# Performance work log

Measured on AMD Instinct MI355X. Metric: run time of the kernel, lower is better.

Reference implementation:

```python
import jax, jax.numpy as jnp
import numpy as np

B, C, L, M, F, N = 4, 32, 256, 256, 8, 64  # N = L // 4 per build()


def setup_inputs() -> dict:
    key = jax.random.key(0)
    k1, k2, k3, k4 = jax.random.split(key, 4)
    return {
        "x_real": jax.random.normal(k1, (B, 1, C, L, M), dtype=jnp.float32),
        "x_imag": jax.random.normal(k2, (B, 1, C, L, M), dtype=jnp.float32),
        "w_real": jax.random.normal(k3, (F, C, N, 1), dtype=jnp.float32),
        "w_imag": jax.random.normal(k4, (F, C, N, 1), dtype=jnp.float32),
    }


def _interp_weights(w, L):
    """tfp.math.interp_regular_1d_grid along axis=-2: map x_targ=0..L-1 over
    ref range [0, L-1] onto an N-point regular grid, linear interpolation."""
    Nn = w.shape[-2]
    t = jnp.arange(L, dtype=jnp.float32) / (L - 1) * (Nn - 1)  # grid coords
    lo = jnp.clip(jnp.floor(t).astype(jnp.int32), 0, Nn - 2)
    frac = (t - lo.astype(jnp.float32))[:, None]               # (L, 1)
    return w[:, :, lo, :] * (1.0 - frac) + w[:, :, lo + 1, :] * frac  # (F,C,L,1)


def reference(x_real, x_imag, w_real, w_imag):
    Lm = x_real.shape[-2]
    wr = _interp_weights(w_real, Lm)  # (F, C, L, 1)
    wi = _interp_weights(w_imag, Lm)
    # complex multiply: (wr + i*wi) * (xr + i*xi), broadcast (B,1,C,L,M)->(B,F,C,L,M)
    pr = wr * x_real - wi * x_imag
    pi = wr * x_imag + wi * x_real
    scale = jnp.sqrt(1.0 + jnp.arange(Lm, dtype=jnp.float32))[:, None]  # self.l, (L,1)
    yr = jnp.mean(pr, axis=-3) * scale  # (B, F, L, M)
    yi = jnp.mean(pi, axis=-3) * scale
    yr = jax.nn.relu(yr)  # relu=True: relu applied to real part only
    return jnp.stack([yr, yi])  # (2, B, F, L, M) == (real, imag)
```

## Files before the change

### kernel.cpp

```cpp
#include <hip/hip_runtime.h>
#include <math.h>

constexpr int B_ = 4, C_ = 32, L_ = 256, M_ = 256, F_ = 8, N_ = 64;

__global__ __launch_bounds__(128, 4) void sphereconv_kernel(
    const float* __restrict__ xr, const float* __restrict__ xi,
    const float* __restrict__ wr, const float* __restrict__ wi,
    float* __restrict__ out)
{
    __shared__ float ws[C_ * 16];

    const int b   = blockIdx.x >> 8;
    const int l   = blockIdx.x & (L_ - 1);
    const int tid = threadIdx.x;

    const float t = ((float)l / (float)(L_ - 1)) * (float)(N_ - 1);
    int lo = (int)floorf(t);
    if (lo > N_ - 2) lo = N_ - 2;
    const float frac = t - (float)lo;

#pragma unroll
    for (int i = tid; i < C_ * 16; i += 128) {
        const int c = i >> 4;
        const int j = i & 15;
        const int f = j & 7;
        const float* w = (j & 8) ? wi : wr;
        const int base = (f * C_ + c) * N_ + lo;
        ws[c * 16 + j] = w[base] * (1.0f - frac) + w[base + 1] * frac;
    }
    __syncthreads();

    float2 accr[F_], acci[F_];
#pragma unroll
    for (int f = 0; f < F_; ++f) {
        accr[f] = make_float2(0.f, 0.f);
        acci[f] = make_float2(0.f, 0.f);
    }

    const size_t strideC2 = (size_t)L_ * M_ / 2;
    const size_t xoff = ((size_t)b * C_) * L_ * M_ + (size_t)l * M_ + tid * 2;
    const float2* xr2 = (const float2*)(xr + xoff);
    const float2* xi2 = (const float2*)(xi + xoff);

#define CX(f, A, Bv)                                          \
    accr[f].x = fmaf(A, vr.x, fmaf(-(Bv), vi.x, accr[f].x));  \
    accr[f].y = fmaf(A, vr.y, fmaf(-(Bv), vi.y, accr[f].y));  \
    acci[f].x = fmaf(A, vi.x, fmaf((Bv), vr.x, acci[f].x));   \
    acci[f].y = fmaf(A, vi.y, fmaf((Bv), vr.y, acci[f].y));

#pragma unroll 4
    for (int c = 0; c < C_; ++c) {
        const float2 vr = xr2[c * strideC2];
        const float2 vi = xi2[c * strideC2];
        const float4 a0 = *(const float4*)&ws[c * 16 + 0];
        const float4 a1 = *(const float4*)&ws[c * 16 + 4];
        const float4 b0 = *(const float4*)&ws[c * 16 + 8];
        const float4 b1 = *(const float4*)&ws[c * 16 + 12];
        CX(0, a0.x, b0.x)
        CX(1, a0.y, b0.y)
        CX(2, a0.z, b0.z)
        CX(3, a0.w, b0.w)
        CX(4, a1.x, b1.x)
        CX(5, a1.y, b1.y)
        CX(6, a1.z, b1.z)
        CX(7, a1.w, b1.w)
    }
#undef CX

    const float scale = sqrtf(1.0f + (float)l) * (1.0f / (float)C_);
    const size_t o0      = (((size_t)b * F_) * L_ + l) * M_ + tid * 2;
    const size_t imagOff = (size_t)B_ * F_ * L_ * M_;
    const size_t fStride = (size_t)L_ * M_;
#pragma unroll
    for (int f = 0; f < F_; ++f) {
        float2 yr, yi;
        yr.x = fmaxf(accr[f].x * scale, 0.f);
        yr.y = fmaxf(accr[f].y * scale, 0.f);
        yi.x = acci[f].x * scale;
        yi.y = acci[f].y * scale;
        *(float2*)(out + o0 + (size_t)f * fStride)           = yr;
        *(float2*)(out + o0 + (size_t)f * fStride + imagOff) = yi;
    }
}

extern "C" void kernel_launch(void* const* d_in, const int* in_sizes, int n_in,
                              void* d_out, int out_size, void* d_ws, size_t ws_size,
                              hipStream_t stream) {
    const float* xr = (const float*)d_in[0];
    const float* xi = (const float*)d_in[1];
    const float* wr = (const float*)d_in[2];
    const float* wi = (const float*)d_in[3];
    float* out = (float*)d_out;
    sphereconv_kernel<<<dim3(B_ * L_), dim3(128), 0, stream>>>(xr, xi, wr, wi, out);
}
```

Baseline: 114.9 us.

## Split channel reduction across two thread groups with shared-memory combine

Doubles the block to 256 threads, with each half of the block accumulating over 16 of the 32 channels. The partial sums are then combined through a 16KB shared-memory buffer before the scaled and ReLU'd outputs are written. The aim is more waves in flight per output row, to hide global load latency on the memory-bound channel loop. In exchange it adds shared-memory traffic, a barrier, and lower occupancy per block from the larger LDS footprint.

```diff
diff --git a/kernel.cpp b/kernel.cpp
--- a/kernel.cpp
+++ b/kernel.cpp
@@ -3,24 +3,27 @@
 
 constexpr int B_ = 4, C_ = 32, L_ = 256, M_ = 256, F_ = 8, N_ = 64;
 
-__global__ __launch_bounds__(128, 4) void sphereconv_kernel(
+__global__ __launch_bounds__(256, 4) void sphereconv_kernel(
     const float* __restrict__ xr, const float* __restrict__ xi,
     const float* __restrict__ wr, const float* __restrict__ wi,
     float* __restrict__ out)
 {
     __shared__ float ws[C_ * 16];
+    __shared__ float red[32 * 128];
 
     const int b   = blockIdx.x >> 8;
     const int l   = blockIdx.x & (L_ - 1);
     const int tid = threadIdx.x;
+    const int grp = tid >> 7;
+    const int t   = tid & 127;
 
-    const float t = ((float)l / (float)(L_ - 1)) * (float)(N_ - 1);
-    int lo = (int)floorf(t);
+    const float tc = ((float)l / (float)(L_ - 1)) * (float)(N_ - 1);
+    int lo = (int)floorf(tc);
     if (lo > N_ - 2) lo = N_ - 2;
-    const float frac = t - (float)lo;
+    const float frac = tc - (float)lo;
 
 #pragma unroll
-    for (int i = tid; i < C_ * 16; i += 128) {
+    for (int i = tid; i < C_ * 16; i += 256) {
         const int c = i >> 4;
         const int j = i & 15;
         const int f = j & 7;
@@ -37,8 +40,9 @@
         acci[f] = make_float2(0.f, 0.f);
     }
 
+    const int c0 = grp * 16;
     const size_t strideC2 = (size_t)L_ * M_ / 2;
-    const size_t xoff = ((size_t)b * C_) * L_ * M_ + (size_t)l * M_ + tid * 2;
+    const size_t xoff = ((size_t)b * C_ + c0) * L_ * M_ + (size_t)l * M_ + t * 2;
     const float2* xr2 = (const float2*)(xr + xoff);
     const float2* xi2 = (const float2*)(xi + xoff);
 
@@ -48,14 +52,15 @@
     acci[f].x = fmaf(A, vi.x, fmaf((Bv), vr.x, acci[f].x));   \
     acci[f].y = fmaf(A, vi.y, fmaf((Bv), vr.y, acci[f].y));
 
-#pragma unroll 4
-    for (int c = 0; c < C_; ++c) {
+#pragma unroll 8
+    for (int c = 0; c < 16; ++c) {
         const float2 vr = xr2[c * strideC2];
         const float2 vi = xi2[c * strideC2];
-        const float4 a0 = *(const float4*)&ws[c * 16 + 0];
-        const float4 a1 = *(const float4*)&ws[c * 16 + 4];
-        const float4 b0 = *(const float4*)&ws[c * 16 + 8];
-        const float4 b1 = *(const float4*)&ws[c * 16 + 12];
+        const float* wp = &ws[(c0 + c) * 16];
+        const float4 a0 = *(const float4*)(wp + 0);
+        const float4 a1 = *(const float4*)(wp + 4);
+        const float4 b0 = *(const float4*)(wp + 8);
+        const float4 b1 = *(const float4*)(wp + 12);
         CX(0, a0.x, b0.x)
         CX(1, a0.y, b0.y)
         CX(2, a0.z, b0.z)
@@ -67,19 +72,31 @@
     }
 #undef CX
 
-    const float scale = sqrtf(1.0f + (float)l) * (1.0f / (float)C_);
-    const size_t o0      = (((size_t)b * F_) * L_ + l) * M_ + tid * 2;
-    const size_t imagOff = (size_t)B_ * F_ * L_ * M_;
-    const size_t fStride = (size_t)L_ * M_;
+    if (grp == 1) {
 #pragma unroll
-    for (int f = 0; f < F_; ++f) {
-        float2 yr, yi;
-        yr.x = fmaxf(accr[f].x * scale, 0.f);
-        yr.y = fmaxf(accr[f].y * scale, 0.f);
-        yi.x = acci[f].x * scale;
-        yi.y = acci[f].y * scale;
-        *(float2*)(out + o0 + (size_t)f * fStride)           = yr;
-        *(float2*)(out + o0 + (size_t)f * fStride + imagOff) = yi;
+        for (int f = 0; f < F_; ++f) {
+            red[(f * 4 + 0) * 128 + t] = accr[f].x;
+            red[(f * 4 + 1) * 128 + t] = accr[f].y;
+            red[(f * 4 + 2) * 128 + t] = acci[f].x;
+            red[(f * 4 + 3) * 128 + t] = acci[f].y;
+        }
+    }
+    __syncthreads();
+    if (grp == 0) {
+        const float scale = sqrtf(1.0f + (float)l) * (1.0f / (float)C_);
+        const size_t o0      = (((size_t)b * F_) * L_ + l) * M_ + t * 2;
+        const size_t imagOff = (size_t)B_ * F_ * L_ * M_;
+        const size_t fStride = (size_t)L_ * M_;
+#pragma unroll
+        for (int f = 0; f < F_; ++f) {
+            float2 yr, yi;
+            yr.x = fmaxf((accr[f].x + red[(f * 4 + 0) * 128 + t]) * scale, 0.f);
+            yr.y = fmaxf((accr[f].y + red[(f * 4 + 1) * 128 + t]) * scale, 0.f);
+            yi.x = (acci[f].x + red[(f * 4 + 2) * 128 + t]) * scale;
+            yi.y = (acci[f].y + red[(f * 4 + 3) * 128 + t]) * scale;
+            *(float2*)(out + o0 + (size_t)f * fStride)           = yr;
+            *(float2*)(out + o0 + (size_t)f * fStride + imagOff) = yi;
+        }
     }
 }
 
@@ -91,5 +108,5 @@
     const float* wr = (const float*)d_in[2];
     const float* wi = (const float*)d_in[3];
     float* out = (float*)d_out;
-    sphereconv_kernel<<<dim3(B_ * L_), dim3(128), 0, stream>>>(xr, xi, wr, wi, out);
+    sphereconv_kernel<<<dim3(B_ * L_), dim3(256), 0, stream>>>(xr, xi, wr, wi, out);
 }
```

Measured after the change: 107.9 us. 6.0% less time.
